# Performance work log

Hardware: AMD Instinct MI355X
Metric: run time of the kernel (lower is better)

## Reference

```python
import jax, jax.numpy as jnp
import numpy as np

N, CIN, C, G, K, H, W = 2, 256, 512, 8, 3, 48, 48
CG = C // G          # channels per group (head dim) = 64
PAD = K // 2
HD, WD = H - K + 1, W - K + 1   # k/v spatial grid (pad=False convs)


def _conv(x, w, groups, pad):
    return jax.lax.conv_general_dilated(
        x, w, window_strides=(1, 1), padding=[(pad, pad), (pad, pad)],
        dimension_numbers=('NCHW', 'OIHW', 'NCHW'), feature_group_count=groups)


def setup_inputs() -> dict:
    key = jax.random.key(0)
    ks = jax.random.split(key, 32)

    def wgt(k, shape):
        fan_in = int(np.prod(shape[1:]))
        return jax.random.normal(k, shape, dtype=jnp.float32) * (fan_in ** -0.5)

    inp = {
        'x_in': jax.random.normal(ks[0], (N, CIN, H, W), dtype=jnp.float32),
        'h':    jax.random.normal(ks[1], (N, C, H, W), dtype=jnp.float32),
        'c':    jax.random.normal(ks[2], (N, C, H, W), dtype=jnp.float32),
        'tau':  jnp.full((G,), CG ** -0.5, dtype=jnp.float32),  # init (channels/groups)^-0.5
        # proj_x: 1x1 from input + intergroup 1x1 on h (groups > 1)
        'W_x':  wgt(ks[3], (C, CIN, 1, 1)),
        'W_ig': wgt(ks[4], (C, C, 1, 1)),
        # grouped KxK q/k/v projections on xh (2C channels, G groups)
        'W_q':  wgt(ks[5], (C, 2 * CG, K, K)),
        'W_k':  wgt(ks[6], (C, 2 * CG, K, K)),
        'W_v':  wgt(ks[7], (C, 2 * CG, K, K)),
    }
    for idx, gate in enumerate(['i', 'f', 'g', 'o']):
        inp[f'W{gate}_a'] = wgt(ks[8 + 3 * idx], (C, CG, 1, 1))        # grouped 1x1 on a
        inp[f'W{gate}_x'] = wgt(ks[9 + 3 * idx], (C, 2 * CG, K, K))    # grouped KxK on xh
        inp[f'b_{gate}'] = jnp.zeros((C,), dtype=jnp.float32)
    return inp


def reference(x_in, h, c, tau, W_x, W_ig, W_q, W_k, W_v,
              Wi_a, Wi_x, b_i, Wf_a, Wf_x, b_f,
              Wg_a, Wg_x, b_g, Wo_a, Wo_x, b_o):
    n = x_in.shape[0]
    # proj_x: sum of 1x1 conv branches (input + intergroup h), no bias
    x = _conv(x_in, W_x, 1, 0) + _conv(h, W_ig, 1, 0)          # [n, C, H, W]

    # xh: per-group interleave of x and h -> [n, 2C, H, W]
    xg = x.reshape(n, G, CG, H, W)
    hg = h.reshape(n, G, CG, H, W)
    xh = jnp.stack([xg, hg], axis=2).reshape(n, 2 * C, H, W)
    # dropout is identity in eval

    q = _conv(xh, W_q, G, PAD).reshape(n, G, CG, H * W)         # [n,G,Cg,Q]
    k = _conv(xh, W_k, G, 0).reshape(n, G, CG, HD * WD)         # [n,G,Cg,D]
    v = _conv(xh, W_v, G, 0).reshape(n, G, CG, HD * WD)

    logits = jnp.einsum('g,ngcq,ngcd->ngqd', tau, q, k)
    w = jax.nn.softmax(logits, axis=3)                          # [n,G,Q,D]
    a = jnp.einsum('ngcd,ngqd->ngcq', v, w).reshape(n, C, H, W)

    def gate(Wa, Wx, b):
        return _conv(a, Wa, G, 0) + _conv(xh, Wx, G, PAD) + b[None, :, None, None]

    i = jax.nn.sigmoid(gate(Wi_a, Wi_x, b_i))
    f = jax.nn.sigmoid(gate(Wf_a, Wf_x, b_f))
    g = jnp.tanh(gate(Wg_a, Wg_x, b_g))
    o = jax.nn.sigmoid(gate(Wo_a, Wo_x, b_o))

    c_new = f * c + i * g
    h_new = o * jnp.tanh(c_new)
    return h_new
```

## Files before the change

kernel.cpp:

```cpp
#include <hip/hip_runtime.h>
#include <hip/hip_bf16.h>
#include <math.h>

#define NB   2
#define CIN  256
#define CC   512
#define GG   8
#define CGR  64
#define HH   48
#define WW   48
#define PP   (HH*WW)
#define HD   46
#define WD   46
#define DD   (HD*WD)
#define DPADV 2120
#define WRT  589824

typedef __bf16 bf16x8 __attribute__((ext_vector_type(8)));
typedef float  f32x4  __attribute__((ext_vector_type(4)));

__device__ __forceinline__ bf16x8 ldb8(const __hip_bfloat16* p) {
    return *reinterpret_cast<const bf16x8*>(p);
}
__device__ __forceinline__ void store4bf(__hip_bfloat16* p, f32x4 v) {
    union { __hip_bfloat16 h[4]; uint2 u; } t;
    #pragma unroll
    for (int r = 0; r < 4; ++r) t.h[r] = (__hip_bfloat16)v[r];
    *reinterpret_cast<uint2*>(p) = t.u;
}
__device__ __forceinline__ float ex2(float x) {
    return __builtin_amdgcn_exp2f(x);
}
__device__ __forceinline__ float sig_fast(float x) {
    return __builtin_amdgcn_rcpf(1.f + ex2(-1.44269504088896f * x));
}
__device__ __forceinline__ float tanh_fast(float x) {
    return 1.f - 2.f * __builtin_amdgcn_rcpf(ex2(2.88539008177793f * x) + 1.f);
}

__global__ __launch_bounds__(256) void prep_kernel(
    const float* __restrict__ Wq, const float* __restrict__ Wk,
    const float* __restrict__ Wv, const float* __restrict__ Wix,
    const float* __restrict__ Wfx, const float* __restrict__ Wgx,
    const float* __restrict__ Wox, const float* __restrict__ Wia,
    const float* __restrict__ Wfa, const float* __restrict__ Wga,
    const float* __restrict__ Woa, const float* __restrict__ Wx,
    const float* __restrict__ Wig,
    __hip_bfloat16* __restrict__ Wr, __hip_bfloat16* __restrict__ Wa,
    __hip_bfloat16* __restrict__ Wp)
{
    const int i = blockIdx.x * 256 + threadIdx.x;
    const int N1 = 7 * WRT;
    const int N2 = N1 + 4 * 32768;
    if (i < N1) {
        const int t = i / WRT, r = i % WRT;
        const int g = r / 73728, r2 = r % 73728;
        const int chunk = r2 / 2048, r3 = r2 % 2048;
        const int och = r3 / 32, k = r3 % 32;
        const int tap = chunk >> 2;
        const int ci = (chunk & 3) * 32 + k;
        const int co = g * 64 + och;
        const float* src;
        switch (t) {
            case 0: src = Wq;  break;  case 1: src = Wk;  break;
            case 2: src = Wv;  break;  case 3: src = Wix; break;
            case 4: src = Wfx; break;  case 5: src = Wgx; break;
            default: src = Wox;
        }
        Wr[i] = (__hip_bfloat16)src[(size_t)co * 1152 + ci * 9 + tap];
    } else if (i < N2) {
        const int j = i - N1;
        const int t = j / 32768, r = j % 32768;
        const float* src = (t == 0) ? Wia : (t == 1) ? Wfa : (t == 2) ? Wga : Woa;
        Wa[j] = (__hip_bfloat16)src[r];
    } else {
        const int j = i - N2;
        const int g = j / 49152, r = j % 49152;
        const int chunk = r / 2048, r3 = r % 2048;
        const int och = r3 / 32, k = r3 % 32;
        const int c = g * 64 + och;
        const int ci = chunk * 32 + k;
        Wp[j] = (__hip_bfloat16)((ci < 256) ? Wx[(size_t)c * 256 + ci]
                                            : Wig[(size_t)c * 512 + (ci - 256)]);
    }
}

__global__ __launch_bounds__(256) void xpose_kernel(
    const float* __restrict__ x_in, const float* __restrict__ h,
    __hip_bfloat16* __restrict__ xiT, __hip_bfloat16* __restrict__ xhT)
{
    const int pt = blockIdx.x;
    const int n  = blockIdx.y;
    const int p0 = pt * 16;
    const int tid = threadIdx.x;

    __shared__ float xs[CIN * 17];
    __shared__ float hs[CC * 17];

    const float* xb = x_in + (size_t)n * CIN * PP;
    const float* hb = h + (size_t)n * CC * PP;
    #pragma unroll
    for (int k = 0; k < 16; ++k) {
        const int idx = k * 256 + tid;
        xs[(idx >> 4) * 17 + (idx & 15)] = xb[(size_t)(idx >> 4) * PP + p0 + (idx & 15)];
    }
    #pragma unroll
    for (int k = 0; k < 32; ++k) {
        const int idx = k * 256 + tid;
        hs[(idx >> 4) * 17 + (idx & 15)] = hb[(size_t)(idx >> 4) * PP + p0 + (idx & 15)];
    }
    __syncthreads();

    #pragma unroll
    for (int it = 0; it < 2; ++it) {
        const int u = it * 256 + tid;
        const int pix = u & 15, ck = u >> 4;
        union { __hip_bfloat16 h8[8]; bf16x8 v; } t;
        #pragma unroll
        for (int j = 0; j < 8; ++j)
            t.h8[j] = (__hip_bfloat16)xs[(ck * 8 + j) * 17 + pix];
        *reinterpret_cast<bf16x8*>(
            xiT + ((size_t)n * PP + p0 + pix) * 256 + ck * 8) = t.v;
    }
    #pragma unroll
    for (int it = 0; it < 4; ++it) {
        const int u = it * 256 + tid;
        const int pix = u & 15, ck = u >> 4;
        const int g = ck >> 3, c8 = (ck & 7) * 8;
        union { __hip_bfloat16 h8[8]; bf16x8 v; } t;
        #pragma unroll
        for (int j = 0; j < 8; ++j)
            t.h8[j] = (__hip_bfloat16)hs[(ck * 8 + j) * 17 + pix];
        *reinterpret_cast<bf16x8*>(
            xhT + ((size_t)(n * GG + g) * PP + p0 + pix) * 128 + 64 + c8) = t.v;
    }
}

__global__ __launch_bounds__(256) void proj_mfma_kernel(
    const __hip_bfloat16* __restrict__ xiT, const __hip_bfloat16* __restrict__ Wp,
    __hip_bfloat16* xhT)
{
    const int b = blockIdx.x;
    const int g = b & 7;
    const int j = b >> 3;
    const int n = j / 12;
    const int yt = j % 12;
    const int ng = n * GG + g;
    const int tid = threadIdx.x;
    const int w = tid >> 6, lane = tid & 63;
    const int col = lane & 15, quad = lane >> 4;
    const int y = yt * 4 + w;

    f32x4 acc[12];
    #pragma unroll
    for (int i = 0; i < 12; ++i) acc[i] = (f32x4){0.f, 0.f, 0.f, 0.f};

    const __hip_bfloat16* wgbase = Wp + (size_t)g * 24 * 2048 + col * 32 + quad * 8;

    for (int kk = 0; kk < 24; ++kk) {
        bf16x8 bfr[3];
        if (kk < 8) {
            const __hip_bfloat16* bp =
                xiT + ((size_t)n * PP + y * 48 + col) * 256 + kk * 32 + quad * 8;
            #pragma unroll
            for (int nf = 0; nf < 3; ++nf)
                bfr[nf] = ldb8(bp + (size_t)(nf * 16) * 256);
        } else {
            const int kh = kk - 8;
            const int gp = kh >> 1;
            const int c0 = (kh & 1) * 32;
            const __hip_bfloat16* bp =
                xhT + ((size_t)(n * GG + gp) * PP + y * 48 + col) * 128 + 64 + c0 + quad * 8;
            #pragma unroll
            for (int nf = 0; nf < 3; ++nf)
                bfr[nf] = ldb8(bp + (size_t)(nf * 16) * 128);
        }
        const __hip_bfloat16* wp = wgbase + kk * 2048;
        #pragma unroll
        for (int cf = 0; cf < 4; ++cf) {
            const bf16x8 af = ldb8(wp + cf * 512);
            #pragma unroll
            for (int nf = 0; nf < 3; ++nf)
                acc[cf * 3 + nf] = __builtin_amdgcn_mfma_f32_16x16x32_bf16(
                    af, bfr[nf], acc[cf * 3 + nf], 0, 0, 0);
        }
    }

    __hip_bfloat16* dst = xhT + (size_t)ng * PP * 128;
    #pragma unroll
    for (int cf = 0; cf < 4; ++cf)
        #pragma unroll
        for (int nf = 0; nf < 3; ++nf) {
            const int pix = y * 48 + nf * 16 + col;
            store4bf(dst + (size_t)pix * 128 + cf * 16 + quad * 4, acc[cf * 3 + nf]);
        }
}

__global__ __launch_bounds__(512) void conv_qkv_kernel(
    const __hip_bfloat16* __restrict__ xhT, const __hip_bfloat16* __restrict__ Wr,
    const float* __restrict__ tau,
    __hip_bfloat16* __restrict__ qT, __hip_bfloat16* __restrict__ kT,
    __hip_bfloat16* __restrict__ v)
{
    const int b = blockIdx.x;
    const int xcd = b & 7;
    const int j = b >> 3;
    const int s = xcd + 8 * (j / 12);
    const int yt = j % 12;
    const int t = s / 16;
    const int ng = s % 16;
    const int g = ng & 7;
    const int tid = threadIdx.x;
    const int w8 = tid >> 6, lane = tid & 63;
    const int yw = w8 & 3, chalf = w8 >> 2;
    const int cf0 = chalf * 2;
    const int col = lane & 15, quad = lane >> 4;
    const int y0 = yt * 4;
    const int yy = y0 + yw;
    const int ohw = (t == 0) ? 48 : 46;
    const int d0 = (t == 0) ? -1 : 0;
    const int soff = (t == 0) ? 1 : 0;
    const bool wave_active = (yy < ohw);

    __shared__ __hip_bfloat16 st[8 * 300 * 8];

    const __hip_bfloat16* slab = xhT + (size_t)ng * PP * 128;
    const __hip_bfloat16* wgbase =
        Wr + ((size_t)t * 8 + g) * 36 * 2048 + col * 32 + quad * 8;

    if (tid < 96) {
        const int ck = tid / 12, r2 = tid % 12;
        const int lr = r2 >> 1, side = r2 & 1;
        const int sc = side ? 49 : (soff ? 0 : 48);
        *reinterpret_cast<bf16x8*>(st + ((ck * 300) + lr * 50 + sc) * 8) =
            (bf16x8)(__bf16)0.f;
    }

    f32x4 acc[6];
    #pragma unroll
    for (int i = 0; i < 6; ++i) acc[i] = (f32x4){0.f, 0.f, 0.f, 0.f};

    for (int hc = 0; hc < 2; ++hc) {
        __syncthreads();
        #pragma unroll
        for (int it = 0; it < 5; ++it) {
            const int u = it * 512 + tid;
            if (u < 2304) {
                const int lr = u / 384;
                const int rem = u % 384;
                const int px = rem >> 3, ck = rem & 7;
                const int ry = y0 + d0 + lr;
                const int ryc = max(0, min(47, ry));
                bf16x8 vv = ldb8(slab + ((size_t)(ryc * 48 + px)) * 128 + hc * 64 + ck * 8);
                *reinterpret_cast<bf16x8*>(st + ((ck * 300) + lr * 50 + px + soff) * 8) =
                    (ry == ryc) ? vv : (bf16x8)(__bf16)0.f;
            }
        }
        __syncthreads();
        if (!wave_active) continue;

        #pragma unroll
        for (int ky = 0; ky < 3; ++ky) {
            const int lrk = (yw + ky) * 50;
            #pragma unroll
            for (int kx = 0; kx < 3; ++kx) {
                const int scb = col + kx;
                #pragma unroll
                for (int c32 = 0; c32 < 2; ++c32) {
                    bf16x8 bfr[3];
                    #pragma unroll
                    for (int nf = 0; nf < 3; ++nf)
                        bfr[nf] = *reinterpret_cast<const bf16x8*>(
                            st + (((c32 * 4 + quad) * 300) + lrk + nf * 16 + scb) * 8);
                    const __hip_bfloat16* wp =
                        wgbase + ((ky * 3 + kx) * 4 + hc * 2 + c32) * 2048;
                    if (t != 2) {
                        #pragma unroll
                        for (int cc = 0; cc < 2; ++cc) {
                            const bf16x8 af = ldb8(wp + (cf0 + cc) * 512);
                            #pragma unroll
                            for (int nf = 0; nf < 3; ++nf)
                                acc[cc * 3 + nf] = __builtin_amdgcn_mfma_f32_16x16x32_bf16(
                                    af, bfr[nf], acc[cc * 3 + nf], 0, 0, 0);
                        }
                    } else {
                        #pragma unroll
                        for (int cc = 0; cc < 2; ++cc) {
                            const bf16x8 af = ldb8(wp + (cf0 + cc) * 512);
                            #pragma unroll
                            for (int nf = 0; nf < 3; ++nf)
                                acc[cc * 3 + nf] = __builtin_amdgcn_mfma_f32_16x16x32_bf16(
                                    bfr[nf], af, acc[cc * 3 + nf], 0, 0, 0);
                        }
                    }
                }
            }
        }
    }

    if (!wave_active) return;
    if (t == 0) {
        const float ts = tau[g] * 1.44269504088896340736f;
        __hip_bfloat16* dst = qT + (size_t)ng * PP * 64;
        #pragma unroll
        for (int cc = 0; cc < 2; ++cc)
            #pragma unroll
            for (int nf = 0; nf < 3; ++nf) {
                const int pix = yy * 48 + nf * 16 + col;
                store4bf(dst + (size_t)pix * 64 + (cf0 + cc) * 16 + quad * 4,
                         acc[cc * 3 + nf] * ts);
            }
    } else if (t == 1) {
        __hip_bfloat16* dst = kT + (size_t)ng * DD * 64;
        #pragma unroll
        for (int cc = 0; cc < 2; ++cc)
            #pragma unroll
            for (int nf = 0; nf < 3; ++nf) {
                const int x = nf * 16 + col;
                if (x < 46) {
                    const int pix = yy * 46 + x;
                    store4bf(dst + (size_t)pix * 64 + (cf0 + cc) * 16 + quad * 4,
                             acc[cc * 3 + nf]);
                }
            }
    } else {
        __hip_bfloat16* dst = v + (size_t)ng * 64 * DPADV;
        #pragma unroll
        for (int cc = 0; cc < 2; ++cc) {
            const int co = (cf0 + cc) * 16 + col;
            #pragma unroll
            for (int nf = 0; nf < 3; ++nf) {
                const int x4 = nf * 16 + quad * 4;
                #pragma unroll
                for (int r = 0; r < 4; ++r) {
                    if (x4 + r < 46)
                        dst[(size_t)co * DPADV + yy * 46 + x4 + r] =
                            (__hip_bfloat16)acc[cc * 3 + nf][r];
                }
            }
        }
    }
}

__global__ __launch_bounds__(256) void attn_kernel(
    __hip_bfloat16* qa,
    const __hip_bfloat16* __restrict__ kT,
    const __hip_bfloat16* __restrict__ vT)
{
    const int idx = blockIdx.x;
    const int j3  = idx >> 3;
    const int sub = (j3 >= 72) ? 1 : 0;
    const int ng  = (idx & 7) + 8 * sub;
    const int qt  = j3 - 72 * sub;
    const int tid = threadIdx.x;
    const int w = tid >> 6, lane = tid & 63;
    const int col = lane & 15, quad = lane >> 4;
    const int qbase = qt * 32;

    const int it0 = w * 17;
    const int it1 = (w < 3) ? (it0 + 17) : 66;

    __shared__ float lmS[3][2][64];
    __shared__ float llS[3][2][64];
    __shared__ float laccS[3][2][64][16];

    __hip_bfloat16* qrowA = qa + ((size_t)ng * PP + qbase + col) * CGR;
    __hip_bfloat16* qrowB = qrowA + 16 * CGR;
    const bf16x8 qfA0 = ldb8(qrowA + quad * 8);
    const bf16x8 qfA1 = ldb8(qrowA + 32 + quad * 8);
    const bf16x8 qfB0 = ldb8(qrowB + quad * 8);
    const bf16x8 qfB1 = ldb8(qrowB + 32 + quad * 8);

    const __hip_bfloat16* kbase = kT + (size_t)ng * DD * CGR;
    const __hip_bfloat16* vbase = vT + (size_t)ng * CGR * DPADV;
    const __hip_bfloat16* vrow[4];
    #pragma unroll
    for (int cf = 0; cf < 4; ++cf)
        vrow[cf] = vbase + (size_t)(cf * 16 + col) * DPADV;

    const int key0 = ((col >> 2) << 3) + (col & 3);
    const __hip_bfloat16* p0 = kbase + (size_t)(it0 * 32 + key0) * CGR + quad * 8;
    const __hip_bfloat16* p1 = p0 + 4 * CGR;

    f32x4 accA[4], accB[4];
    #pragma unroll
    for (int cf = 0; cf < 4; ++cf) {
        accA[cf] = (f32x4){0.f, 0.f, 0.f, 0.f};
        accB[cf] = (f32x4){0.f, 0.f, 0.f, 0.f};
    }
    float mA = -INFINITY, mB = -INFINITY;
    float lA = 0.f, lB = 0.f;
    const f32x4 zero = {0.f, 0.f, 0.f, 0.f};

    for (int it = it0; it < it1; ++it) {
        const int dbase = it * 32;
        const bf16x8 K0a = ldb8(p0), K0b = ldb8(p0 + 32);
        const bf16x8 K1a = ldb8(p1), K1b = ldb8(p1 + 32);
        p0 += 32 * CGR; p1 += 32 * CGR;

        f32x4 SA0 = __builtin_amdgcn_mfma_f32_16x16x32_bf16(K0a, qfA0, zero, 0, 0, 0);
        SA0 = __builtin_amdgcn_mfma_f32_16x16x32_bf16(K0b, qfA1, SA0, 0, 0, 0);
        f32x4 SA1 = __builtin_amdgcn_mfma_f32_16x16x32_bf16(K1a, qfA0, zero, 0, 0, 0);
        SA1 = __builtin_amdgcn_mfma_f32_16x16x32_bf16(K1b, qfA1, SA1, 0, 0, 0);
        f32x4 SB0 = __builtin_amdgcn_mfma_f32_16x16x32_bf16(K0a, qfB0, zero, 0, 0, 0);
        SB0 = __builtin_amdgcn_mfma_f32_16x16x32_bf16(K0b, qfB1, SB0, 0, 0, 0);
        f32x4 SB1 = __builtin_amdgcn_mfma_f32_16x16x32_bf16(K1a, qfB0, zero, 0, 0, 0);
        SB1 = __builtin_amdgcn_mfma_f32_16x16x32_bf16(K1b, qfB1, SB1, 0, 0, 0);

        const int da = dbase + quad * 8;
        const bf16x8 vf0 = ldb8(vrow[0] + da);
        const bf16x8 vf1 = ldb8(vrow[1] + da);
        const bf16x8 vf2 = ldb8(vrow[2] + da);
        const bf16x8 vf3 = ldb8(vrow[3] + da);

        const float lmAx = fmaxf(fmaxf(fmaxf(SA0[0], SA0[1]), fmaxf(SA0[2], SA0[3])),
                                 fmaxf(fmaxf(SA1[0], SA1[1]), fmaxf(SA1[2], SA1[3])));
        const float lmBx = fmaxf(fmaxf(fmaxf(SB0[0], SB0[1]), fmaxf(SB0[2], SB0[3])),
                                 fmaxf(fmaxf(SB1[0], SB1[1]), fmaxf(SB1[2], SB1[3])));

        if (__any((lmAx > mA + 8.f) || (lmBx > mB + 8.f))) {
            float sA = lmAx;
            sA = fmaxf(sA, __shfl_xor(sA, 16, 64));
            sA = fmaxf(sA, __shfl_xor(sA, 32, 64));
            float sB = lmBx;
            sB = fmaxf(sB, __shfl_xor(sB, 16, 64));
            sB = fmaxf(sB, __shfl_xor(sB, 32, 64));
            const float mnA = fmaxf(mA, sA), mnB = fmaxf(mB, sB);
            const float aA = ex2(mA - mnA), aB = ex2(mB - mnB);
            lA *= aA; lB *= aB;
            #pragma unroll
            for (int cf = 0; cf < 4; ++cf) { accA[cf] *= aA; accB[cf] *= aB; }
            mA = mnA; mB = mnB;
        }

        float eA[8], eB[8];
        float lsA = 0.f, lsB = 0.f;
        #pragma unroll
        for (int r = 0; r < 4; ++r) {
            eA[r]     = ex2(SA0[r] - mA);
            eA[4 + r] = ex2(SA1[r] - mA);
            eB[r]     = ex2(SB0[r] - mB);
            eB[4 + r] = ex2(SB1[r] - mB);
            lsA += eA[r] + eA[4 + r];
            lsB += eB[r] + eB[4 + r];
        }
        lA += lsA; lB += lsB;

        bf16x8 ptA, ptB;
        #pragma unroll
        for (int jj = 0; jj < 8; ++jj) { ptA[jj] = (__bf16)eA[jj]; ptB[jj] = (__bf16)eB[jj]; }

        accA[0] = __builtin_amdgcn_mfma_f32_16x16x32_bf16(vf0, ptA, accA[0], 0, 0, 0);
        accB[0] = __builtin_amdgcn_mfma_f32_16x16x32_bf16(vf0, ptB, accB[0], 0, 0, 0);
        accA[1] = __builtin_amdgcn_mfma_f32_16x16x32_bf16(vf1, ptA, accA[1], 0, 0, 0);
        accB[1] = __builtin_amdgcn_mfma_f32_16x16x32_bf16(vf1, ptB, accB[1], 0, 0, 0);
        accA[2] = __builtin_amdgcn_mfma_f32_16x16x32_bf16(vf2, ptA, accA[2], 0, 0, 0);
        accB[2] = __builtin_amdgcn_mfma_f32_16x16x32_bf16(vf2, ptB, accB[2], 0, 0, 0);
        accA[3] = __builtin_amdgcn_mfma_f32_16x16x32_bf16(vf3, ptA, accA[3], 0, 0, 0);
        accB[3] = __builtin_amdgcn_mfma_f32_16x16x32_bf16(vf3, ptB, accB[3], 0, 0, 0);
    }

    if (w == 3) {
        const int dbase = 66 * 32;
        const int kk0 = min(dbase + key0, DD - 1);
        const int kk1 = min(dbase + key0 + 4, DD - 1);
        const __hip_bfloat16* t0 = kbase + (size_t)kk0 * CGR + quad * 8;
        const __hip_bfloat16* t1 = kbase + (size_t)kk1 * CGR + quad * 8;
        const bf16x8 Ka = ldb8(t0), Kb = ldb8(t0 + 32);
        const bf16x8 Kc = ldb8(t1), Kd = ldb8(t1 + 32);

        f32x4 SA0 = __builtin_amdgcn_mfma_f32_16x16x32_bf16(Ka, qfA0, zero, 0, 0, 0);
        SA0 = __builtin_amdgcn_mfma_f32_16x16x32_bf16(Kb, qfA1, SA0, 0, 0, 0);
        f32x4 SA1 = __builtin_amdgcn_mfma_f32_16x16x32_bf16(Kc, qfA0, zero, 0, 0, 0);
        SA1 = __builtin_amdgcn_mfma_f32_16x16x32_bf16(Kd, qfA1, SA1, 0, 0, 0);
        f32x4 SB0 = __builtin_amdgcn_mfma_f32_16x16x32_bf16(Ka, qfB0, zero, 0, 0, 0);
        SB0 = __builtin_amdgcn_mfma_f32_16x16x32_bf16(Kb, qfB1, SB0, 0, 0, 0);
        f32x4 SB1 = __builtin_amdgcn_mfma_f32_16x16x32_bf16(Kc, qfB0, zero, 0, 0, 0);
        SB1 = __builtin_amdgcn_mfma_f32_16x16x32_bf16(Kd, qfB1, SB1, 0, 0, 0);

        float eA[8], eB[8];
        #pragma unroll
        for (int r = 0; r < 4; ++r) {
            const bool v0 = (dbase + quad * 8 + r     < DD);
            const bool v1 = (dbase + quad * 8 + 4 + r < DD);
            eA[r]     = v0 ? SA0[r] : -1e30f;
            eA[4 + r] = v1 ? SA1[r] : -1e30f;
            eB[r]     = v0 ? SB0[r] : -1e30f;
            eB[4 + r] = v1 ? SB1[r] : -1e30f;
        }
        float sA = fmaxf(fmaxf(fmaxf(eA[0], eA[1]), fmaxf(eA[2], eA[3])),
                         fmaxf(fmaxf(eA[4], eA[5]), fmaxf(eA[6], eA[7])));
        sA = fmaxf(sA, __shfl_xor(sA, 16, 64));
        sA = fmaxf(sA, __shfl_xor(sA, 32, 64));
        float sB = fmaxf(fmaxf(fmaxf(eB[0], eB[1]), fmaxf(eB[2], eB[3])),
                         fmaxf(fmaxf(eB[4], eB[5]), fmaxf(eB[6], eB[7])));
        sB = fmaxf(sB, __shfl_xor(sB, 16, 64));
        sB = fmaxf(sB, __shfl_xor(sB, 32, 64));
        const float mnA = fmaxf(mA, sA), mnB = fmaxf(mB, sB);
        const float aA = ex2(mA - mnA), aB = ex2(mB - mnB);
        float lsA = 0.f, lsB = 0.f;
        #pragma unroll
        for (int jj = 0; jj < 8; ++jj) {
            eA[jj] = ex2(eA[jj] - mnA); lsA += eA[jj];
            eB[jj] = ex2(eB[jj] - mnB); lsB += eB[jj];
        }
        lA = lA * aA + lsA;
        lB = lB * aB + lsB;
        mA = mnA; mB = mnB;

        bf16x8 ptA, ptB;
        #pragma unroll
        for (int jj = 0; jj < 8; ++jj) { ptA[jj] = (__bf16)eA[jj]; ptB[jj] = (__bf16)eB[jj]; }

        int da = dbase + quad * 8;
        if (da >= DD) da = 0;
        #pragma unroll
        for (int cf = 0; cf < 4; ++cf) {
            accA[cf] *= aA; accB[cf] *= aB;
            const bf16x8 vf = ldb8(vrow[cf] + da);
            accA[cf] = __builtin_amdgcn_mfma_f32_16x16x32_bf16(vf, ptA, accA[cf], 0, 0, 0);
            accB[cf] = __builtin_amdgcn_mfma_f32_16x16x32_bf16(vf, ptB, accB[cf], 0, 0, 0);
        }
    }

    if (w != 0) {
        lmS[w - 1][0][lane] = mA; lmS[w - 1][1][lane] = mB;
        llS[w - 1][0][lane] = lA; llS[w - 1][1][lane] = lB;
        #pragma unroll
        for (int cf = 0; cf < 4; ++cf) {
            *reinterpret_cast<f32x4*>(&laccS[w - 1][0][lane][cf * 4]) = accA[cf];
            *reinterpret_cast<f32x4*>(&laccS[w - 1][1][lane][cf * 4]) = accB[cf];
        }
    }
    __syncthreads();
    if (w != 0) return;

    #pragma unroll
    for (int ww = 0; ww < 3; ++ww) {
        {
            const float mo = lmS[ww][0][lane];
            const float lo = llS[ww][0][lane];
            const float mn = fmaxf(mA, mo);
            const float a0 = ex2(mA - mn);
            const float a1 = ex2(mo - mn);
            lA = lA * a0 + lo * a1;
            #pragma unroll
            for (int cf = 0; cf < 4; ++cf) {
                const f32x4 o = *reinterpret_cast<const f32x4*>(&laccS[ww][0][lane][cf * 4]);
                accA[cf] = accA[cf] * a0 + o * a1;
            }
            mA = mn;
        }
        {
            const float mo = lmS[ww][1][lane];
            const float lo = llS[ww][1][lane];
            const float mn = fmaxf(mB, mo);
            const float a0 = ex2(mB - mn);
            const float a1 = ex2(mo - mn);
            lB = lB * a0 + lo * a1;
            #pragma unroll
            for (int cf = 0; cf < 4; ++cf) {
                const f32x4 o = *reinterpret_cast<const f32x4*>(&laccS[ww][1][lane][cf * 4]);
                accB[cf] = accB[cf] * a0 + o * a1;
            }
            mB = mn;
        }
    }

    lA += __shfl_xor(lA, 16, 64);
    lA += __shfl_xor(lA, 32, 64);
    lB += __shfl_xor(lB, 16, 64);
    lB += __shfl_xor(lB, 32, 64);

    const float invA = 1.f / lA;
    const float invB = 1.f / lB;
    #pragma unroll
    for (int cf = 0; cf < 4; ++cf) {
        store4bf(qrowA + cf * 16 + quad * 4, accA[cf] * invA);
        store4bf(qrowB + cf * 16 + quad * 4, accB[cf] * invB);
    }
}

__global__ __launch_bounds__(512) void gates_kernel(
    const __hip_bfloat16* __restrict__ xhT, const __hip_bfloat16* __restrict__ aT,
    const float* __restrict__ c_in,
    const __hip_bfloat16* __restrict__ Wr, const __hip_bfloat16* __restrict__ Wa,
    const float* __restrict__ b_i, const float* __restrict__ b_f,
    const float* __restrict__ b_g, const float* __restrict__ b_o,
    float* __restrict__ h_out)
{
    const int b = blockIdx.x;
    const int xcd = b & 7;
    const int j = b >> 3;
    const int ng = xcd + 8 * (j / 48);
    const int yy = j % 48;
    const int n = ng >> 3, g = ng & 7;
    const int tid = threadIdx.x;
    const int w8 = tid >> 6, lane = tid & 63;
    const int gate = w8 & 3, chalf = w8 >> 2;
    const int cf0 = chalf * 2;
    const int col = lane & 15, quad = lane >> 4;

    __shared__ char smem[38400];
    __hip_bfloat16* st = (__hip_bfloat16*)smem;
    float* ex = (float*)smem;

    const __hip_bfloat16* slab = xhT + (size_t)ng * PP * 128;

    if (tid < 96) {
        const int ck = tid / 6, r2 = tid % 6;
        const int lr = r2 >> 1, side = r2 & 1;
        const int sc = side ? 49 : 0;
        *reinterpret_cast<bf16x8*>(st + ((ck * 150) + lr * 50 + sc) * 8) =
            (bf16x8)(__bf16)0.f;
    }
    #pragma unroll
    for (int it = 0; it < 5; ++it) {
        const int u = it * 512 + tid;
        if (u < 2304) {
            const int lr = u / 768;
            const int rem = u % 768;
            const int px = rem >> 4, ck = rem & 15;
            const int ry = yy - 1 + lr;
            const int ryc = max(0, min(47, ry));
            bf16x8 vv = ldb8(slab + ((size_t)(ryc * 48 + px)) * 128 + ck * 8);
            *reinterpret_cast<bf16x8*>(st + ((ck * 150) + lr * 50 + px + 1) * 8) =
                (ry == ryc) ? vv : (bf16x8)(__bf16)0.f;
        }
    }
    __syncthreads();

    f32x4 acc[6];
    #pragma unroll
    for (int i = 0; i < 6; ++i) acc[i] = (f32x4){0.f, 0.f, 0.f, 0.f};

    const __hip_bfloat16* wgbase =
        Wr + ((size_t)(3 + gate) * 8 + g) * 36 * 2048 + col * 32 + quad * 8;

    #pragma unroll
    for (int ky = 0; ky < 3; ++ky) {
        const int lrk = ky * 50;
        #pragma unroll
        for (int kx = 0; kx < 3; ++kx) {
            const int scb = col + kx;
            #pragma unroll
            for (int c32 = 0; c32 < 4; ++c32) {
                bf16x8 bfr[3];
                #pragma unroll
                for (int nf = 0; nf < 3; ++nf)
                    bfr[nf] = *reinterpret_cast<const bf16x8*>(
                        st + (((c32 * 4 + quad) * 150) + lrk + nf * 16 + scb) * 8);
                const __hip_bfloat16* wp =
                    wgbase + ((ky * 3 + kx) * 4 + c32) * 2048;
                #pragma unroll
                for (int cc = 0; cc < 2; ++cc) {
                    const bf16x8 af = ldb8(wp + (cf0 + cc) * 512);
                    #pragma unroll
                    for (int nf = 0; nf < 3; ++nf)
                        acc[cc * 3 + nf] = __builtin_amdgcn_mfma_f32_16x16x32_bf16(
                            af, bfr[nf], acc[cc * 3 + nf], 0, 0, 0);
                }
            }
        }
    }

    {
        const __hip_bfloat16* wa =
            Wa + (size_t)gate * 32768 + ((size_t)(g * 64) + col) * 64;
        const __hip_bfloat16* ab = aT + ((size_t)ng * PP + yy * 48) * 64;
        #pragma unroll
        for (int c32 = 0; c32 < 2; ++c32) {
            bf16x8 bfr[3];
            #pragma unroll
            for (int nf = 0; nf < 3; ++nf)
                bfr[nf] = ldb8(ab + (size_t)(nf * 16 + col) * 64 + c32 * 32 + quad * 8);
            #pragma unroll
            for (int cc = 0; cc < 2; ++cc) {
                const bf16x8 af = ldb8(wa + (size_t)((cf0 + cc) * 16) * 64 + c32 * 32 + quad * 8);
                #pragma unroll
                for (int nf = 0; nf < 3; ++nf)
                    acc[cc * 3 + nf] = __builtin_amdgcn_mfma_f32_16x16x32_bf16(
                        af, bfr[nf], acc[cc * 3 + nf], 0, 0, 0);
            }
        }
    }

    const float* bias = (gate == 0) ? b_i : (gate == 1) ? b_f : (gate == 2) ? b_g : b_o;
    #pragma unroll
    for (int cc = 0; cc < 2; ++cc) {
        #pragma unroll
        for (int r = 0; r < 4; ++r) {
            const float bv = bias[g * 64 + (cf0 + cc) * 16 + quad * 4 + r];
            #pragma unroll
            for (int nf = 0; nf < 3; ++nf)
                acc[cc * 3 + nf][r] += bv;
        }
    }

    for (int hh = 0; hh < 2; ++hh) {
        __syncthreads();
        if (chalf == hh) {
            #pragma unroll
            for (int cc = 0; cc < 2; ++cc)
                #pragma unroll
                for (int nf = 0; nf < 3; ++nf)
                    #pragma unroll
                    for (int r = 0; r < 4; ++r)
                        ex[(size_t)gate * 1536 + (cc * 16 + quad * 4 + r) * 48 + nf * 16 + col] =
                            acc[cc * 3 + nf][r];
        }
        __syncthreads();
        #pragma unroll
        for (int k2 = 0; k2 < 3; ++k2) {
            const int idx = k2 * 512 + tid;
            const int co32 = idx / 48, px = idx % 48;
            const float iv = ex[0 * 1536 + co32 * 48 + px];
            const float fv = ex[1 * 1536 + co32 * 48 + px];
            const float gv = ex[2 * 1536 + co32 * 48 + px];
            const float ov = ex[3 * 1536 + co32 * 48 + px];
            const int c = g * 64 + hh * 32 + co32;
            const size_t off = ((size_t)n * CC + c) * PP + yy * 48 + px;
            const float ig = sig_fast(iv);
            const float fg = sig_fast(fv);
            const float gg = tanh_fast(gv);
            const float og = sig_fast(ov);
            const float cn = fg * c_in[off] + ig * gg;
            h_out[off] = og * tanh_fast(cn);
        }
    }
}

extern "C" void kernel_launch(void* const* d_in, const int* in_sizes, int n_in,
                              void* d_out, int out_size, void* d_ws, size_t ws_size,
                              hipStream_t stream)
{
    const float* x_in = (const float*)d_in[0];
    const float* h    = (const float*)d_in[1];
    const float* c    = (const float*)d_in[2];
    const float* tau  = (const float*)d_in[3];
    const float* W_x  = (const float*)d_in[4];
    const float* W_ig = (const float*)d_in[5];
    const float* W_q  = (const float*)d_in[6];
    const float* W_k  = (const float*)d_in[7];
    const float* W_v  = (const float*)d_in[8];
    const float* Wi_a = (const float*)d_in[9];
    const float* Wi_x = (const float*)d_in[10];
    const float* b_i  = (const float*)d_in[11];
    const float* Wf_a = (const float*)d_in[12];
    const float* Wf_x = (const float*)d_in[13];
    const float* b_f  = (const float*)d_in[14];
    const float* Wg_a = (const float*)d_in[15];
    const float* Wg_x = (const float*)d_in[16];
    const float* b_g  = (const float*)d_in[17];
    const float* Wo_a = (const float*)d_in[18];
    const float* Wo_x = (const float*)d_in[19];
    const float* b_o  = (const float*)d_in[20];
    float* out = (float*)d_out;

    __hip_bfloat16* wsb = (__hip_bfloat16*)d_ws;
    __hip_bfloat16* xhT = wsb;
    __hip_bfloat16* qa  = xhT + (size_t)4718592;
    __hip_bfloat16* kT  = qa  + (size_t)2359296;
    __hip_bfloat16* vv  = kT  + (size_t)2166784;
    __hip_bfloat16* Wr  = vv  + (size_t)2170880;
    __hip_bfloat16* Wa  = Wr  + (size_t)4128768;
    __hip_bfloat16* Wp  = Wa  + (size_t)131072;
    __hip_bfloat16* xiT = Wp  + (size_t)393216;

    dim3 blk(256);
    dim3 blk8(512);
    prep_kernel<<<dim3(18176), blk, 0, stream>>>(
        W_q, W_k, W_v, Wi_x, Wf_x, Wg_x, Wo_x, Wi_a, Wf_a, Wg_a, Wo_a,
        W_x, W_ig, Wr, Wa, Wp);
    xpose_kernel<<<dim3(144, NB), blk, 0, stream>>>(x_in, h, xiT, xhT);
    proj_mfma_kernel<<<dim3(192), blk, 0, stream>>>(xiT, Wp, xhT);
    conv_qkv_kernel<<<dim3(576), blk8, 0, stream>>>(xhT, Wr, tau, qa, kT, vv);
    attn_kernel<<<dim3(1152), blk, 0, stream>>>(qa, kT, vv);
    gates_kernel<<<dim3(768), blk8, 0, stream>>>(
        xhT, qa, c, Wr, Wa, b_i, b_f, b_g, b_o, out);
}
```

Measured before the change: 284.4 us.

## Halve attention query tile to 16 rows, double grid, and prefetch K fragments

The attention kernel now gives each block 16 queries instead of 32, so the grid doubles to 2304 blocks and each wave holds one query fragment set instead of two. It also software-prefetches the next iteration's K fragments into registers before the current QK MFMAs run. The intent is more parallelism and lower register pressure, plus hiding K-load latency. The cost is that K and V are read twice as often overall, since each block now amortizes them over half as many queries.

```diff
diff --git a/kernel.cpp b/kernel.cpp
--- a/kernel.cpp
+++ b/kernel.cpp
@@ -349,27 +349,24 @@
 {
     const int idx = blockIdx.x;
     const int j3  = idx >> 3;
-    const int sub = (j3 >= 72) ? 1 : 0;
+    const int sub = (j3 >= 144) ? 1 : 0;
     const int ng  = (idx & 7) + 8 * sub;
-    const int qt  = j3 - 72 * sub;
+    const int qt  = j3 - 144 * sub;
     const int tid = threadIdx.x;
     const int w = tid >> 6, lane = tid & 63;
     const int col = lane & 15, quad = lane >> 4;
-    const int qbase = qt * 32;
+    const int qbase = qt * 16;
 
     const int it0 = w * 17;
     const int it1 = (w < 3) ? (it0 + 17) : 66;
 
-    __shared__ float lmS[3][2][64];
-    __shared__ float llS[3][2][64];
-    __shared__ float laccS[3][2][64][16];
-
-    __hip_bfloat16* qrowA = qa + ((size_t)ng * PP + qbase + col) * CGR;
-    __hip_bfloat16* qrowB = qrowA + 16 * CGR;
-    const bf16x8 qfA0 = ldb8(qrowA + quad * 8);
-    const bf16x8 qfA1 = ldb8(qrowA + 32 + quad * 8);
-    const bf16x8 qfB0 = ldb8(qrowB + quad * 8);
-    const bf16x8 qfB1 = ldb8(qrowB + 32 + quad * 8);
+    __shared__ float lmS[3][64];
+    __shared__ float llS[3][64];
+    __shared__ float laccS[3][64][16];
+
+    __hip_bfloat16* qrow = qa + ((size_t)ng * PP + qbase + col) * CGR;
+    const bf16x8 qf0 = ldb8(qrow + quad * 8);
+    const bf16x8 qf1 = ldb8(qrow + 32 + quad * 8);
 
     const __hip_bfloat16* kbase = kT + (size_t)ng * DD * CGR;
     const __hip_bfloat16* vbase = vT + (size_t)ng * CGR * DPADV;
@@ -382,30 +379,29 @@
     const __hip_bfloat16* p0 = kbase + (size_t)(it0 * 32 + key0) * CGR + quad * 8;
     const __hip_bfloat16* p1 = p0 + 4 * CGR;
 
-    f32x4 accA[4], accB[4];
-    #pragma unroll
-    for (int cf = 0; cf < 4; ++cf) {
-        accA[cf] = (f32x4){0.f, 0.f, 0.f, 0.f};
-        accB[cf] = (f32x4){0.f, 0.f, 0.f, 0.f};
-    }
-    float mA = -INFINITY, mB = -INFINITY;
-    float lA = 0.f, lB = 0.f;
+    f32x4 acc[4];
+    #pragma unroll
+    for (int cf = 0; cf < 4; ++cf) acc[cf] = (f32x4){0.f, 0.f, 0.f, 0.f};
+    float m = -INFINITY;
+    float l = 0.f;
     const f32x4 zero = {0.f, 0.f, 0.f, 0.f};
+
+    bf16x8 A0 = ldb8(p0), A1 = ldb8(p0 + 32);
+    bf16x8 B0 = ldb8(p1), B1 = ldb8(p1 + 32);
 
     for (int it = it0; it < it1; ++it) {
         const int dbase = it * 32;
-        const bf16x8 K0a = ldb8(p0), K0b = ldb8(p0 + 32);
-        const bf16x8 K1a = ldb8(p1), K1b = ldb8(p1 + 32);
         p0 += 32 * CGR; p1 += 32 * CGR;
-
-        f32x4 SA0 = __builtin_amdgcn_mfma_f32_16x16x32_bf16(K0a, qfA0, zero, 0, 0, 0);
-        SA0 = __builtin_amdgcn_mfma_f32_16x16x32_bf16(K0b, qfA1, SA0, 0, 0, 0);
-        f32x4 SA1 = __builtin_amdgcn_mfma_f32_16x16x32_bf16(K1a, qfA0, zero, 0, 0, 0);
-        SA1 = __builtin_amdgcn_mfma_f32_16x16x32_bf16(K1b, qfA1, SA1, 0, 0, 0);
-        f32x4 SB0 = __builtin_amdgcn_mfma_f32_16x16x32_bf16(K0a, qfB0, zero, 0, 0, 0);
-        SB0 = __builtin_amdgcn_mfma_f32_16x16x32_bf16(K0b, qfB1, SB0, 0, 0, 0);
-        f32x4 SB1 = __builtin_amdgcn_mfma_f32_16x16x32_bf16(K1a, qfB0, zero, 0, 0, 0);
-        SB1 = __builtin_amdgcn_mfma_f32_16x16x32_bf16(K1b, qfB1, SB1, 0, 0, 0);
+        bf16x8 nA0, nA1, nB0, nB1;
+        if (it + 1 < it1) {
+            nA0 = ldb8(p0); nA1 = ldb8(p0 + 32);
+            nB0 = ldb8(p1); nB1 = ldb8(p1 + 32);
+        }
+
+        f32x4 S0 = __builtin_amdgcn_mfma_f32_16x16x32_bf16(A0, qf0, zero, 0, 0, 0);
+        S0 = __builtin_amdgcn_mfma_f32_16x16x32_bf16(A1, qf1, S0, 0, 0, 0);
+        f32x4 S1 = __builtin_amdgcn_mfma_f32_16x16x32_bf16(B0, qf0, zero, 0, 0, 0);
+        S1 = __builtin_amdgcn_mfma_f32_16x16x32_bf16(B1, qf1, S1, 0, 0, 0);
 
         const int da = dbase + quad * 8;
         const bf16x8 vf0 = ldb8(vrow[0] + da);
@@ -413,51 +409,41 @@
         const bf16x8 vf2 = ldb8(vrow[2] + da);
         const bf16x8 vf3 = ldb8(vrow[3] + da);
 
-        const float lmAx = fmaxf(fmaxf(fmaxf(SA0[0], SA0[1]), fmaxf(SA0[2], SA0[3])),
-                                 fmaxf(fmaxf(SA1[0], SA1[1]), fmaxf(SA1[2], SA1[3])));
-        const float lmBx = fmaxf(fmaxf(fmaxf(SB0[0], SB0[1]), fmaxf(SB0[2], SB0[3])),
-                                 fmaxf(fmaxf(SB1[0], SB1[1]), fmaxf(SB1[2], SB1[3])));
-
-        if (__any((lmAx > mA + 8.f) || (lmBx > mB + 8.f))) {
-            float sA = lmAx;
-            sA = fmaxf(sA, __shfl_xor(sA, 16, 64));
-            sA = fmaxf(sA, __shfl_xor(sA, 32, 64));
-            float sB = lmBx;
-            sB = fmaxf(sB, __shfl_xor(sB, 16, 64));
-            sB = fmaxf(sB, __shfl_xor(sB, 32, 64));
-            const float mnA = fmaxf(mA, sA), mnB = fmaxf(mB, sB);
-            const float aA = ex2(mA - mnA), aB = ex2(mB - mnB);
-            lA *= aA; lB *= aB;
-            #pragma unroll
-            for (int cf = 0; cf < 4; ++cf) { accA[cf] *= aA; accB[cf] *= aB; }
-            mA = mnA; mB = mnB;
-        }
-
-        float eA[8], eB[8];
-        float lsA = 0.f, lsB = 0.f;
+        const float lmx = fmaxf(fmaxf(fmaxf(S0[0], S0[1]), fmaxf(S0[2], S0[3])),
+                                fmaxf(fmaxf(S1[0], S1[1]), fmaxf(S1[2], S1[3])));
+
+        if (__any(lmx > m + 8.f)) {
+            float s = lmx;
+            s = fmaxf(s, __shfl_xor(s, 16, 64));
+            s = fmaxf(s, __shfl_xor(s, 32, 64));
+            const float mn = fmaxf(m, s);
+            const float a = ex2(m - mn);
+            l *= a;
+            #pragma unroll
+            for (int cf = 0; cf < 4; ++cf) acc[cf] *= a;
+            m = mn;
+        }
+
+        float e[8];
+        float lsum = 0.f;
         #pragma unroll
         for (int r = 0; r < 4; ++r) {
-            eA[r]     = ex2(SA0[r] - mA);
-            eA[4 + r] = ex2(SA1[r] - mA);
-            eB[r]     = ex2(SB0[r] - mB);
-            eB[4 + r] = ex2(SB1[r] - mB);
-            lsA += eA[r] + eA[4 + r];
-            lsB += eB[r] + eB[4 + r];
-        }
-        lA += lsA; lB += lsB;
-
-        bf16x8 ptA, ptB;
-        #pragma unroll
-        for (int jj = 0; jj < 8; ++jj) { ptA[jj] = (__bf16)eA[jj]; ptB[jj] = (__bf16)eB[jj]; }
-
-        accA[0] = __builtin_amdgcn_mfma_f32_16x16x32_bf16(vf0, ptA, accA[0], 0, 0, 0);
-        accB[0] = __builtin_amdgcn_mfma_f32_16x16x32_bf16(vf0, ptB, accB[0], 0, 0, 0);
-        accA[1] = __builtin_amdgcn_mfma_f32_16x16x32_bf16(vf1, ptA, accA[1], 0, 0, 0);
-        accB[1] = __builtin_amdgcn_mfma_f32_16x16x32_bf16(vf1, ptB, accB[1], 0, 0, 0);
-        accA[2] = __builtin_amdgcn_mfma_f32_16x16x32_bf16(vf2, ptA, accA[2], 0, 0, 0);
-        accB[2] = __builtin_amdgcn_mfma_f32_16x16x32_bf16(vf2, ptB, accB[2], 0, 0, 0);
-        accA[3] = __builtin_amdgcn_mfma_f32_16x16x32_bf16(vf3, ptA, accA[3], 0, 0, 0);
-        accB[3] = __builtin_amdgcn_mfma_f32_16x16x32_bf16(vf3, ptB, accB[3], 0, 0, 0);
+            e[r]     = ex2(S0[r] - m);
+            e[4 + r] = ex2(S1[r] - m);
+            lsum += e[r] + e[4 + r];
+        }
+        l += lsum;
+
+        bf16x8 pt;
+        #pragma unroll
+        for (int jj = 0; jj < 8; ++jj) pt[jj] = (__bf16)e[jj];
+
+        acc[0] = __builtin_amdgcn_mfma_f32_16x16x32_bf16(vf0, pt, acc[0], 0, 0, 0);
+        acc[1] = __builtin_amdgcn_mfma_f32_16x16x32_bf16(vf1, pt, acc[1], 0, 0, 0);
+        acc[2] = __builtin_amdgcn_mfma_f32_16x16x32_bf16(vf2, pt, acc[2], 0, 0, 0);
+        acc[3] = __builtin_amdgcn_mfma_f32_16x16x32_bf16(vf3, pt, acc[3], 0, 0, 0);
+
+        A0 = nA0; A1 = nA1; B0 = nB0; B1 = nB1;
     }
 
     if (w == 3) {
@@ -466,119 +452,76 @@
         const int kk1 = min(dbase + key0 + 4, DD - 1);
         const __hip_bfloat16* t0 = kbase + (size_t)kk0 * CGR + quad * 8;
         const __hip_bfloat16* t1 = kbase + (size_t)kk1 * CGR + quad * 8;
-        const bf16x8 Ka = ldb8(t0), Kb = ldb8(t0 + 32);
-        const bf16x8 Kc = ldb8(t1), Kd = ldb8(t1 + 32);
-
-        f32x4 SA0 = __builtin_amdgcn_mfma_f32_16x16x32_bf16(Ka, qfA0, zero, 0, 0, 0);
-        SA0 = __builtin_amdgcn_mfma_f32_16x16x32_bf16(Kb, qfA1, SA0, 0, 0, 0);
-        f32x4 SA1 = __builtin_amdgcn_mfma_f32_16x16x32_bf16(Kc, qfA0, zero, 0, 0, 0);
-        SA1 = __builtin_amdgcn_mfma_f32_16x16x32_bf16(Kd, qfA1, SA1, 0, 0, 0);
-        f32x4 SB0 = __builtin_amdgcn_mfma_f32_16x16x32_bf16(Ka, qfB0, zero, 0, 0, 0);
-        SB0 = __builtin_amdgcn_mfma_f32_16x16x32_bf16(Kb, qfB1, SB0, 0, 0, 0);
-        f32x4 SB1 = __builtin_amdgcn_mfma_f32_16x16x32_bf16(Kc, qfB0, zero, 0, 0, 0);
-        SB1 = __builtin_amdgcn_mfma_f32_16x16x32_bf16(Kd, qfB1, SB1, 0, 0, 0);
-
-        float eA[8], eB[8];
+        f32x4 S0 = __builtin_amdgcn_mfma_f32_16x16x32_bf16(ldb8(t0), qf0, zero, 0, 0, 0);
+        S0 = __builtin_amdgcn_mfma_f32_16x16x32_bf16(ldb8(t0 + 32), qf1, S0, 0, 0, 0);
+        f32x4 S1 = __builtin_amdgcn_mfma_f32_16x16x32_bf16(ldb8(t1), qf0, zero, 0, 0, 0);
+        S1 = __builtin_amdgcn_mfma_f32_16x16x32_bf16(ldb8(t1 + 32), qf1, S1, 0, 0, 0);
+
+        float e[8];
         #pragma unroll
         for (int r = 0; r < 4; ++r) {
-            const bool v0 = (dbase + quad * 8 + r     < DD);
-            const bool v1 = (dbase + quad * 8 + 4 + r < DD);
-            eA[r]     = v0 ? SA0[r] : -1e30f;
-            eA[4 + r] = v1 ? SA1[r] : -1e30f;
-            eB[r]     = v0 ? SB0[r] : -1e30f;
-            eB[4 + r] = v1 ? SB1[r] : -1e30f;
-        }
-        float sA = fmaxf(fmaxf(fmaxf(eA[0], eA[1]), fmaxf(eA[2], eA[3])),
-                         fmaxf(fmaxf(eA[4], eA[5]), fmaxf(eA[6], eA[7])));
-        sA = fmaxf(sA, __shfl_xor(sA, 16, 64));
-        sA = fmaxf(sA, __shfl_xor(sA, 32, 64));
-        float sB = fmaxf(fmaxf(fmaxf(eB[0], eB[1]), fmaxf(eB[2], eB[3])),
-                         fmaxf(fmaxf(eB[4], eB[5]), fmaxf(eB[6], eB[7])));
-        sB = fmaxf(sB, __shfl_xor(sB, 16, 64));
-        sB = fmaxf(sB, __shfl_xor(sB, 32, 64));
-        const float mnA = fmaxf(mA, sA), mnB = fmaxf(mB, sB);
-        const float aA = ex2(mA - mnA), aB = ex2(mB - mnB);
-        float lsA = 0.f, lsB = 0.f;
-        #pragma unroll
-        for (int jj = 0; jj < 8; ++jj) {
-            eA[jj] = ex2(eA[jj] - mnA); lsA += eA[jj];
-            eB[jj] = ex2(eB[jj] - mnB); lsB += eB[jj];
-        }
-        lA = lA * aA + lsA;
-        lB = lB * aB + lsB;
-        mA = mnA; mB = mnB;
-
-        bf16x8 ptA, ptB;
-        #pragma unroll
-        for (int jj = 0; jj < 8; ++jj) { ptA[jj] = (__bf16)eA[jj]; ptB[jj] = (__bf16)eB[jj]; }
+            e[r]     = (dbase + quad * 8 + r     < DD) ? S0[r] : -1e30f;
+            e[4 + r] = (dbase + quad * 8 + 4 + r < DD) ? S1[r] : -1e30f;
+        }
+        float s = fmaxf(fmaxf(fmaxf(e[0], e[1]), fmaxf(e[2], e[3])),
+                        fmaxf(fmaxf(e[4], e[5]), fmaxf(e[6], e[7])));
+        s = fmaxf(s, __shfl_xor(s, 16, 64));
+        s = fmaxf(s, __shfl_xor(s, 32, 64));
+        const float mn = fmaxf(m, s);
+        const float a = ex2(m - mn);
+        float lsum = 0.f;
+        #pragma unroll
+        for (int jj = 0; jj < 8; ++jj) { e[jj] = ex2(e[jj] - mn); lsum += e[jj]; }
+        l = l * a + lsum;
+        m = mn;
+
+        bf16x8 pt;
+        #pragma unroll
+        for (int jj = 0; jj < 8; ++jj) pt[jj] = (__bf16)e[jj];
 
         int da = dbase + quad * 8;
         if (da >= DD) da = 0;
         #pragma unroll
         for (int cf = 0; cf < 4; ++cf) {
-            accA[cf] *= aA; accB[cf] *= aB;
-            const bf16x8 vf = ldb8(vrow[cf] + da);
-            accA[cf] = __builtin_amdgcn_mfma_f32_16x16x32_bf16(vf, ptA, accA[cf], 0, 0, 0);
-            accB[cf] = __builtin_amdgcn_mfma_f32_16x16x32_bf16(vf, ptB, accB[cf], 0, 0, 0);
+            acc[cf] *= a;
+            acc[cf] = __builtin_amdgcn_mfma_f32_16x16x32_bf16(
+                ldb8(vrow[cf] + da), pt, acc[cf], 0, 0, 0);
         }
     }
 
     if (w != 0) {
-        lmS[w - 1][0][lane] = mA; lmS[w - 1][1][lane] = mB;
-        llS[w - 1][0][lane] = lA; llS[w - 1][1][lane] = lB;
-        #pragma unroll
-        for (int cf = 0; cf < 4; ++cf) {
-            *reinterpret_cast<f32x4*>(&laccS[w - 1][0][lane][cf * 4]) = accA[cf];
-            *reinterpret_cast<f32x4*>(&laccS[w - 1][1][lane][cf * 4]) = accB[cf];
-        }
+        lmS[w - 1][lane] = m;
+        llS[w - 1][lane] = l;
+        #pragma unroll
+        for (int cf = 0; cf < 4; ++cf)
+            *reinterpret_cast<f32x4*>(&laccS[w - 1][lane][cf * 4]) = acc[cf];
     }
     __syncthreads();
     if (w != 0) return;
 
     #pragma unroll
     for (int ww = 0; ww < 3; ++ww) {
-        {
-            const float mo = lmS[ww][0][lane];
-            const float lo = llS[ww][0][lane];
-            const float mn = fmaxf(mA, mo);
-            const float a0 = ex2(mA - mn);
-            const float a1 = ex2(mo - mn);
-            lA = lA * a0 + lo * a1;
-            #pragma unroll
-            for (int cf = 0; cf < 4; ++cf) {
-                const f32x4 o = *reinterpret_cast<const f32x4*>(&laccS[ww][0][lane][cf * 4]);
-                accA[cf] = accA[cf] * a0 + o * a1;
-            }
-            mA = mn;
-        }
-        {
-            const float mo = lmS[ww][1][lane];
-            const float lo = llS[ww][1][lane];
-            const float mn = fmaxf(mB, mo);
-            const float a0 = ex2(mB - mn);
-            const float a1 = ex2(mo - mn);
-            lB = lB * a0 + lo * a1;
-            #pragma unroll
-            for (int cf = 0; cf < 4; ++cf) {
-                const f32x4 o = *reinterpret_cast<const f32x4*>(&laccS[ww][1][lane][cf * 4]);
-                accB[cf] = accB[cf] * a0 + o * a1;
-            }
-            mB = mn;
-        }
-    }
-
-    lA += __shfl_xor(lA, 16, 64);
-    lA += __shfl_xor(lA, 32, 64);
-    lB += __shfl_xor(lB, 16, 64);
-    lB += __shfl_xor(lB, 32, 64);
-
-    const float invA = 1.f / lA;
-    const float invB = 1.f / lB;
-    #pragma unroll
-    for (int cf = 0; cf < 4; ++cf) {
-        store4bf(qrowA + cf * 16 + quad * 4, accA[cf] * invA);
-        store4bf(qrowB + cf * 16 + quad * 4, accB[cf] * invB);
-    }
+        const float mo = lmS[ww][lane];
+        const float lo = llS[ww][lane];
+        const float mn = fmaxf(m, mo);
+        const float a0 = ex2(m - mn);
+        const float a1 = ex2(mo - mn);
+        l = l * a0 + lo * a1;
+        #pragma unroll
+        for (int cf = 0; cf < 4; ++cf) {
+            const f32x4 o = *reinterpret_cast<const f32x4*>(&laccS[ww][lane][cf * 4]);
+            acc[cf] = acc[cf] * a0 + o * a1;
+        }
+        m = mn;
+    }
+
+    l += __shfl_xor(l, 16, 64);
+    l += __shfl_xor(l, 32, 64);
+
+    const float inv = 1.f / l;
+    #pragma unroll
+    for (int cf = 0; cf < 4; ++cf)
+        store4bf(qrow + cf * 16 + quad * 4, acc[cf] * inv);
 }
 
 __global__ __launch_bounds__(512) void gates_kernel(
@@ -775,7 +718,7 @@
     xpose_kernel<<<dim3(144, NB), blk, 0, stream>>>(x_in, h, xiT, xhT);
     proj_mfma_kernel<<<dim3(192), blk, 0, stream>>>(xiT, Wp, xhT);
     conv_qkv_kernel<<<dim3(576), blk8, 0, stream>>>(xhT, Wr, tau, qa, kT, vv);
-    attn_kernel<<<dim3(1152), blk, 0, stream>>>(qa, kT, vv);
+    attn_kernel<<<dim3(2304), blk, 0, stream>>>(qa, kT, vv);
     gates_kernel<<<dim3(768), blk8, 0, stream>>>(
         xhT, qa, c, Wr, Wa, b_i, b_f, b_g, b_o, out);
 }
```

Result: slower. 324.8 us (+14.2%).
